# Optimization experiments

Hardware: AMD Instinct MI355X
Metric: run time of the kernel (lower is better)

## Reference

```python
import jax, jax.numpy as jnp
import numpy as np

H = 256        # hidden_channels
G = 13         # num_input_geofeature
E = 100000     # number of 2nd-order triplets
N = 50000      # num_nodes
DEPTH = 3      # finaldepth
EPS = 1e-5     # BatchNorm eps


def setup_inputs() -> dict:
    key = jax.random.key(0)
    ks = jax.random.split(key, 10)
    d_in = 3 * H + G  # 781
    return {
        "node_feature": jax.random.normal(ks[0], (N, H), jnp.float32),
        "geo_encoding": jax.random.normal(ks[1], (E, G), jnp.float32),
        "edge_index_2rd": jax.random.randint(ks[2], (3, E), 0, N),
        "edx_ij": jax.random.randint(ks[3], (E,), 0, 2 * E),
        "edx_jk": jax.random.randint(ks[4], (E,), 0, 2 * E),
        "att": jax.random.uniform(ks[5], (4,), jnp.float32),
        # 4 branches: layer0 (d_in->H) + DEPTH layers (H->H), xavier-ish init, zero bias
        "W0": jax.random.normal(ks[6], (4, d_in, H), jnp.float32) * (1.0 / np.sqrt(d_in)),
        "b0": jnp.zeros((4, H), jnp.float32),
        "Wh": jax.random.normal(ks[7], (4, DEPTH, H, H), jnp.float32) * (1.0 / np.sqrt(H)),
        "bh": jnp.zeros((4, DEPTH, H), jnp.float32),
        # BatchNorm (eval mode): affine params + running stats, one per layer per branch
        "gamma": jnp.ones((4, DEPTH + 1, H), jnp.float32),
        "beta": jnp.zeros((4, DEPTH + 1, H), jnp.float32),
        "run_mean": jnp.zeros((4, DEPTH + 1, H), jnp.float32),
        "run_var": jnp.ones((4, DEPTH + 1, H), jnp.float32),
        "num_edge_inside": E,
        "num_nodes": N,
    }


def _bn(h, g, b, m, v):
    return (h - m) * jax.lax.rsqrt(v + EPS) * g + b


def reference(node_feature, geo_encoding, edge_index_2rd, edx_ij, edx_jk, att,
              W0, b0, Wh, bh, gamma, beta, run_mean, run_var,
              num_edge_inside, num_nodes):
    i, j, k = edge_index_2rd[0], edge_index_2rd[1], edge_index_2rd[2]
    # gather node triplets + geo features -> [E, 3H+G]
    x = jnp.concatenate(
        [node_feature[i], node_feature[j], node_feature[k], geo_encoding], axis=-1)

    m_ij = edx_ij < num_edge_inside
    m_jk = edx_jk < num_edge_inside
    # 4 mutually-exclusive, exhaustive routing masks: [4, E]
    masks = jnp.stack([m_ij & m_jk, m_ij & ~m_jk, ~m_ij & m_jk, ~m_ij & ~m_jk])

    x_output = jnp.zeros((x.shape[0], H), x.dtype)
    for br in range(4):  # fixed small branch count
        h = jax.nn.relu(_bn(x @ W0[br] + b0[br],
                            gamma[br, 0], beta[br, 0], run_mean[br, 0], run_var[br, 0]))
        for l in range(DEPTH):
            h = jax.nn.relu(_bn(h @ Wh[br, l] + bh[br, l],
                                gamma[br, l + 1], beta[br, l + 1],
                                run_mean[br, l + 1], run_var[br, l + 1]))
        h = jax.nn.leaky_relu(h) * att[br]
        x_output = x_output + jnp.where(masks[br][:, None], h, jnp.zeros((), h.dtype))
    # scatter_add over target node index i -> [num_nodes, H]
    return jax.ops.segment_sum(x_output, i, num_segments=num_nodes)
```

## Files before the change

### kernel.cpp

```cpp
#include <hip/hip_runtime.h>
#include <hip/hip_bf16.h>
#include <stdint.h>

#define HCH 256
#define GEO 13
#define DEPTH 3
#define EPSBN 1e-5f
#define MFMA __builtin_amdgcn_mfma_f32_16x16x32_bf16

typedef __attribute__((ext_vector_type(8))) short short8;
typedef __attribute__((ext_vector_type(4))) float floatx4;

__device__ __forceinline__ short f2bs(float f) {
    unsigned u = __float_as_uint(f);
    unsigned r = (u + 0x7fffu + ((u >> 16) & 1u)) >> 16;
    return (short)r;
}

__global__ void k_prep(const float* __restrict__ W0, const float* __restrict__ Wh,
                       const float* __restrict__ b0, const float* __restrict__ bh,
                       const float* __restrict__ gm, const float* __restrict__ bt,
                       const float* __restrict__ mn, const float* __restrict__ vr,
                       const float* __restrict__ att,
                       const float* __restrict__ node, const float* __restrict__ geo,
                       const int* __restrict__ edx_ij, const int* __restrict__ edx_jk,
                       const int* __restrict__ nei_p,
                       short* __restrict__ W0t, short* __restrict__ Wht,
                       float* __restrict__ sc, float* __restrict__ of,
                       short* __restrict__ node_bf, short* __restrict__ geo_bf,
                       int* __restrict__ lists, int* __restrict__ cnt,
                       float4* __restrict__ outz, int n4out,
                       int E, int d_in_dim, int nb_node, int nb_geo, int nb_out) {
    const int B_W0 = 100, B_WH = 96, B_SC = 16;
    __shared__ short s[32][256];
    int b = blockIdx.x, t = threadIdx.x;
    if (b < B_W0) {
        int c = b % 25, br = b / 25;
        #pragma unroll
        for (int kk = 0; kk < 32; ++kk) {
            int kidx = c * 32 + kk;
            float v = (kidx < d_in_dim) ? W0[((size_t)br * d_in_dim + kidx) * HCH + t] : 0.f;
            s[kk][t] = f2bs(v);
        }
        __syncthreads();
        size_t obase = ((size_t)(b) * 256 + t) * 32;
        #pragma unroll
        for (int g = 0; g < 4; ++g) {
            short8 v;
            #pragma unroll
            for (int j = 0; j < 8; ++j) v[j] = s[g * 8 + j][t];
            *reinterpret_cast<short8*>(W0t + obase + g * 8) = v;
        }
    } else if (b < B_W0 + B_WH) {
        int idx = b - B_W0;
        int c = idx & 7; idx >>= 3;
        int l = idx % 3, br = idx / 3;
        #pragma unroll
        for (int kk = 0; kk < 32; ++kk) {
            float v = Wh[((size_t)(br * DEPTH + l) * HCH + (c * 32 + kk)) * HCH + t];
            s[kk][t] = f2bs(v);
        }
        __syncthreads();
        size_t obase = ((size_t)(b - B_W0) * 256 + t) * 32;
        #pragma unroll
        for (int g = 0; g < 4; ++g) {
            short8 v;
            #pragma unroll
            for (int j = 0; j < 8; ++j) v[j] = s[g * 8 + j][t];
            *reinterpret_cast<short8*>(Wht + obase + g * 8) = v;
        }
    } else if (b < B_W0 + B_WH + B_SC) {
        int idx = (b - B_W0 - B_WH) * 256 + t;
        int col = idx & 255, l = (idx >> 8) & 3, br = idx >> 10;
        int gi = (br * (DEPTH + 1) + l) * HCH + col;
        float sA = gm[gi] * rsqrtf(vr[gi] + EPSBN);
        float bias = (l == 0) ? b0[br * HCH + col] : bh[(br * DEPTH + (l - 1)) * HCH + col];
        float ofv = (bias - mn[gi]) * sA + bt[gi];
        if (l == 3) { float av = att[br]; sA *= av; ofv *= av; }
        sc[idx] = sA;
        of[idx] = ofv;
    } else if (b < B_W0 + B_WH + B_SC + nb_node) {
        size_t i = ((size_t)(b - B_W0 - B_WH - B_SC) * 256 + t) * 8;
        const float4* src = reinterpret_cast<const float4*>(node + i);
        float4 v0 = src[0], v1 = src[1];
        short8 pk;
        pk[0] = f2bs(v0.x); pk[1] = f2bs(v0.y); pk[2] = f2bs(v0.z); pk[3] = f2bs(v0.w);
        pk[4] = f2bs(v1.x); pk[5] = f2bs(v1.y); pk[6] = f2bs(v1.z); pk[7] = f2bs(v1.w);
        *reinterpret_cast<short8*>(node_bf + i) = pk;
    } else if (b < B_W0 + B_WH + B_SC + nb_node + nb_geo) {
        int i = (b - B_W0 - B_WH - B_SC - nb_node) * 256 + t;
        int e = i >> 2, cc = i & 3;
        if (e < E) {
            short8 pk;
            #pragma unroll
            for (int j = 0; j < 8; ++j) {
                int col = cc * 8 + j;
                pk[j] = (col < GEO) ? f2bs(geo[(size_t)e * GEO + col]) : (short)0;
            }
            *reinterpret_cast<short8*>(geo_bf + (size_t)e * 32 + cc * 8) = pk;
        }
    } else if (b < B_W0 + B_WH + B_SC + nb_node + nb_geo + nb_out) {
        int i = (b - (B_W0 + B_WH + B_SC + nb_node + nb_geo)) * 256 + t;
        if (i < n4out) outz[i] = make_float4(0.f, 0.f, 0.f, 0.f);
    } else {
        int e = (b - (B_W0 + B_WH + B_SC + nb_node + nb_geo + nb_out)) * 256 + t;
        int NEI = nei_p[0];
        int lane = t & 63;
        int br = -1;
        if (e < E)
            br = ((edx_ij[e] < NEI) ? 0 : 2) + ((edx_jk[e] < NEI) ? 0 : 1);
        unsigned long long lt = (lane == 63) ? 0x7fffffffffffffffull
                                             : ((1ull << lane) - 1ull);
        #pragma unroll
        for (int bb = 0; bb < 4; ++bb) {
            unsigned long long mk = __ballot(br == bb);
            if (mk) {
                int leader = __ffsll((long long)mk) - 1;
                int base = 0;
                if (lane == leader) base = atomicAdd(&cnt[bb], (int)__popcll(mk));
                base = __shfl(base, leader);
                if (br == bb) {
                    int pos = base + (int)__popcll(mk & lt);
                    lists[(size_t)bb * E + pos] = e;
                }
            }
        }
    }
}

__global__ __launch_bounds__(512)
void k_main(const short* __restrict__ node_bf, const short* __restrict__ geo_bf,
            const int* __restrict__ eidx,
            const short* __restrict__ W0t, const short* __restrict__ Wht,
            const float* __restrict__ sc, const float* __restrict__ of,
            const int* __restrict__ lists, const int* __restrict__ cnt,
            float* __restrict__ out, int E) {
    __shared__ __align__(16) short A[64][256];
    __shared__ __align__(16) short Ageo[64][40];
    __shared__ int s_idx[3][64];
    __shared__ int s_e[64];

    int c0 = cnt[0], c1 = cnt[1], c2 = cnt[2], c3 = cnt[3];
    int t0 = (c0 + 63) >> 6, t1 = (c1 + 63) >> 6, t2 = (c2 + 63) >> 6, t3 = (c3 + 63) >> 6;
    int b = blockIdx.x;
    int br, tile, count;
    if (b < t0)                     { br = 0; tile = b;                count = c0; }
    else if (b < t0 + t1)           { br = 1; tile = b - t0;           count = c1; }
    else if (b < t0 + t1 + t2)      { br = 2; tile = b - t0 - t1;      count = c2; }
    else if (b < t0 + t1 + t2 + t3) { br = 3; tile = b - t0 - t1 - t2; count = c3; }
    else return;
    int m = count - tile * 64; if (m > 64) m = 64;

    int t = threadIdx.x;
    if (t < 64) {
        int e = (t < m) ? lists[(size_t)br * E + (size_t)tile * 64 + t] : 0;
        s_e[t] = (t < m) ? e : -1;
        s_idx[0][t] = eidx[e];
        s_idx[1][t] = eidx[E + e];
        s_idx[2][t] = eidx[2 * E + e];
    }
    __syncthreads();

    int wv = t >> 6, lane = t & 63, quad = lane >> 4, l16 = lane & 15;
    int rbase = t >> 5, cc8 = (t & 31) * 8;
    int swz = (l16 & 7) << 4;

    floatx4 acc[4][2];
    #pragma unroll
    for (int rt = 0; rt < 4; ++rt)
        #pragma unroll
        for (int ct = 0; ct < 2; ++ct)
            #pragma unroll
            for (int r = 0; r < 4; ++r) acc[rt][ct][r] = 0.f;

    int boff[2];
    #pragma unroll
    for (int ct = 0; ct < 2; ++ct)
        boff[ct] = (wv * 32 + ct * 16 + l16) * 32 + quad * 8;

    const char* Ab = (const char*)&A[0][0];
    char* Aw = (char*)&A[0][0];
    short* Ag = &Ageo[0][0];

    auto do_chunks8 = [&](const short* Wbase) {
        short8 bb[4][2];
        #pragma unroll
        for (int s = 0; s < 3; ++s)
            #pragma unroll
            for (int ct = 0; ct < 2; ++ct)
                bb[s][ct] = *reinterpret_cast<const short8*>(
                    Wbase + (size_t)s * 8192 + boff[ct]);
        #pragma unroll
        for (int c = 0; c < 8; ++c) {
            if (c + 3 < 8) {
                const short* Bn = Wbase + (size_t)(c + 3) * 8192;
                #pragma unroll
                for (int ct = 0; ct < 2; ++ct)
                    bb[(c + 3) & 3][ct] = *reinterpret_cast<const short8*>(Bn + boff[ct]);
            }
            short8 af[4];
            #pragma unroll
            for (int rt = 0; rt < 4; ++rt)
                af[rt] = *reinterpret_cast<const short8*>(
                    Ab + (rt * 16 + l16) * 512 + ((c * 64 + quad * 16) ^ swz));
            __builtin_amdgcn_s_setprio(1);
            #pragma unroll
            for (int rt = 0; rt < 4; ++rt)
                #pragma unroll
                for (int ct = 0; ct < 2; ++ct)
                    acc[rt][ct] = MFMA(af[rt], bb[c & 3][ct], acc[rt][ct], 0, 0, 0);
            __builtin_amdgcn_s_setprio(0);
        }
    };
    auto do_chunk1 = [&](const short* Wbase) {
        short8 bc[2];
        #pragma unroll
        for (int ct = 0; ct < 2; ++ct)
            bc[ct] = *reinterpret_cast<const short8*>(Wbase + boff[ct]);
        short8 af[4];
        #pragma unroll
        for (int rt = 0; rt < 4; ++rt)
            af[rt] = *reinterpret_cast<const short8*>(
                Ag + (rt * 16 + l16) * 40 + quad * 8);
        __builtin_amdgcn_s_setprio(1);
        #pragma unroll
        for (int rt = 0; rt < 4; ++rt)
            #pragma unroll
            for (int ct = 0; ct < 2; ++ct)
                acc[rt][ct] = MFMA(af[rt], bc[ct], acc[rt][ct], 0, 0, 0);
        __builtin_amdgcn_s_setprio(0);
    };

    if (t < 256) {
        int grow = t >> 2, gp = (t & 3) * 8;
        int ge = s_e[grow];
        short8 gv;
        if (ge >= 0) gv = *reinterpret_cast<const short8*>(geo_bf + (size_t)ge * 32 + gp);
        else {
            #pragma unroll
            for (int j = 0; j < 8; ++j) gv[j] = 0;
        }
        *reinterpret_cast<short8*>(Ag + grow * 40 + gp) = gv;
    }
    short8 g[2][4];
    #pragma unroll
    for (int it = 0; it < 4; ++it)
        g[0][it] = *reinterpret_cast<const short8*>(
            node_bf + (size_t)s_idx[0][it * 16 + rbase] * HCH + cc8);

    #pragma unroll
    for (int p = 0; p < 3; ++p) {
        __syncthreads();
        #pragma unroll
        for (int it = 0; it < 4; ++it) {
            int row = it * 16 + rbase;
            *reinterpret_cast<short8*>(
                Aw + row * 512 + ((cc8 * 2) ^ ((row & 7) << 4))) = g[p & 1][it];
        }
        __syncthreads();
        if (p < 2) {
            const int* idxs = s_idx[p + 1];
            #pragma unroll
            for (int it = 0; it < 4; ++it)
                g[(p + 1) & 1][it] = *reinterpret_cast<const short8*>(
                    node_bf + (size_t)idxs[it * 16 + rbase] * HCH + cc8);
        }
        do_chunks8(W0t + (size_t)(br * 25 + p * 8) * 8192);
    }
    do_chunk1(W0t + (size_t)(br * 25 + 24) * 8192);

    for (int l = 0; l < 4; ++l) {
        float sv[2], ov[2];
        #pragma unroll
        for (int ct = 0; ct < 2; ++ct) {
            int col = wv * 32 + ct * 16 + l16;
            sv[ct] = sc[(br * 4 + l) * HCH + col];
            ov[ct] = of[(br * 4 + l) * HCH + col];
        }
        if (l < 3) {
            __syncthreads();
            #pragma unroll
            for (int rt = 0; rt < 4; ++rt)
                #pragma unroll
                for (int ct = 0; ct < 2; ++ct) {
                    int colb = (wv * 32 + ct * 16 + l16) * 2;
                    #pragma unroll
                    for (int r = 0; r < 4; ++r) {
                        int row = rt * 16 + quad * 4 + r;
                        float h = fmaxf(acc[rt][ct][r] * sv[ct] + ov[ct], 0.f);
                        *reinterpret_cast<short*>(
                            Aw + row * 512 + (colb ^ ((row & 7) << 4))) = f2bs(h);
                        acc[rt][ct][r] = 0.f;
                    }
                }
            __syncthreads();
            do_chunks8(Wht + (size_t)((br * 3 + l) * 8) * 8192);
        } else {
            #pragma unroll
            for (int rt = 0; rt < 4; ++rt)
                #pragma unroll
                for (int r = 0; r < 4; ++r) {
                    int row = rt * 16 + quad * 4 + r;
                    if (row < m) {
                        float* orow = out + (size_t)s_idx[0][row] * HCH + wv * 32 + l16;
                        #pragma unroll
                        for (int ct = 0; ct < 2; ++ct) {
                            float h = fmaxf(acc[rt][ct][r] * sv[ct] + ov[ct], 0.f);
                            atomicAdd(orow + ct * 16, h);
                        }
                    }
                }
        }
    }
}

extern "C" void kernel_launch(void* const* d_in, const int* in_sizes, int n_in,
                              void* d_out, int out_size, void* d_ws, size_t ws_size,
                              hipStream_t stream) {
    const float* node  = (const float*)d_in[0];
    const float* geo   = (const float*)d_in[1];
    const int*   eidx  = (const int*)d_in[2];
    const int*   edxij = (const int*)d_in[3];
    const int*   edxjk = (const int*)d_in[4];
    const float* att   = (const float*)d_in[5];
    const float* W0    = (const float*)d_in[6];
    const float* b0    = (const float*)d_in[7];
    const float* Wh    = (const float*)d_in[8];
    const float* bh    = (const float*)d_in[9];
    const float* gm    = (const float*)d_in[10];
    const float* bt    = (const float*)d_in[11];
    const float* mn    = (const float*)d_in[12];
    const float* vr    = (const float*)d_in[13];
    const int*   neip  = (const int*)d_in[14];

    int E = in_sizes[3];
    int N = in_sizes[0] / HCH;
    int d_in_dim = in_sizes[6] / (4 * HCH);

    uint8_t* w = (uint8_t*)d_ws;
    size_t off = 0;
    short* W0t  = (short*)(w + off); off += (size_t)4 * 25 * 256 * 32 * 2;
    short* Wht  = (short*)(w + off); off += (size_t)4 * 3 * 8 * 256 * 32 * 2;
    float* sc   = (float*)(w + off); off += 4096 * 4;
    float* of   = (float*)(w + off); off += 4096 * 4;
    int*   lists= (int*)(w + off);   off += (size_t)4 * E * 4;
    int*   cnt  = (int*)(w + off);   off += 16;
    short* node_bf = (short*)(w + off); off += (size_t)N * HCH * 2;
    short* geo_bf  = (short*)(w + off); off += (size_t)E * 32 * 2;

    float* out = (float*)d_out;
    int n4 = out_size / 4;

    hipMemsetAsync(cnt, 0, 16, stream);

    int nb_node = N / 8;
    int nb_geo  = (4 * E + 255) / 256;
    int nb_out  = (n4 + 255) / 256;
    int nb_cmp  = (E + 255) / 256;
    k_prep<<<100 + 96 + 16 + nb_node + nb_geo + nb_out + nb_cmp, 256, 0, stream>>>(
        W0, Wh, b0, bh, gm, bt, mn, vr, att, node, geo, edxij, edxjk, neip,
        W0t, Wht, sc, of, node_bf, geo_bf, lists, cnt,
        (float4*)out, n4, E, d_in_dim, nb_node, nb_geo, nb_out);

    int T = (E >> 6) + 8;
    k_main<<<T, 512, 0, stream>>>(node_bf, geo_bf, eidx, W0t, Wht,
                                  sc, of, lists, cnt, out, E);
}
```

Measured before the change: 409.4 us.

## Pad LDS rows instead of XOR swizzle, remap blocks per XCD, trim prefetch

Replaces the XOR-swizzled shared-memory layout for the activation tile with a padded row stride of 264 shorts. Block IDs are remapped so that consecutive logical tiles land on the same XCD, which is meant to improve L2 locality for weights and branch data. The weight prefetch depth in the chunk loop drops from three to two buffers, and the MFMA priority hints are removed. Padding adds a little LDS, and the shallower prefetch may expose more global load latency.

New measurement: 393.7 us. 1.04x faster.

```diff
diff --git a/kernel.cpp b/kernel.cpp
--- a/kernel.cpp
+++ b/kernel.cpp
@@ -135,14 +135,18 @@
             const float* __restrict__ sc, const float* __restrict__ of,
             const int* __restrict__ lists, const int* __restrict__ cnt,
             float* __restrict__ out, int E) {
-    __shared__ __align__(16) short A[64][256];
+    __shared__ __align__(16) short A[64][264];
     __shared__ __align__(16) short Ageo[64][40];
     __shared__ int s_idx[3][64];
     __shared__ int s_e[64];
 
+    int nwg = gridDim.x;
+    int q = nwg >> 3, r = nwg & 7;
+    int xcd = blockIdx.x & 7, jj = blockIdx.x >> 3;
+    int b = ((xcd < r) ? xcd * (q + 1) : r * (q + 1) + (xcd - r) * q) + jj;
+
     int c0 = cnt[0], c1 = cnt[1], c2 = cnt[2], c3 = cnt[3];
     int t0 = (c0 + 63) >> 6, t1 = (c1 + 63) >> 6, t2 = (c2 + 63) >> 6, t3 = (c3 + 63) >> 6;
-    int b = blockIdx.x;
     int br, tile, count;
     if (b < t0)                     { br = 0; tile = b;                count = c0; }
     else if (b < t0 + t1)           { br = 1; tile = b - t0;           count = c1; }
@@ -163,7 +167,6 @@
 
     int wv = t >> 6, lane = t & 63, quad = lane >> 4, l16 = lane & 15;
     int rbase = t >> 5, cc8 = (t & 31) * 8;
-    int swz = (l16 & 7) << 4;
 
     floatx4 acc[4][2];
     #pragma unroll
@@ -171,45 +174,39 @@
         #pragma unroll
         for (int ct = 0; ct < 2; ++ct)
             #pragma unroll
-            for (int r = 0; r < 4; ++r) acc[rt][ct][r] = 0.f;
+            for (int r2 = 0; r2 < 4; ++r2) acc[rt][ct][r2] = 0.f;
 
     int boff[2];
     #pragma unroll
     for (int ct = 0; ct < 2; ++ct)
         boff[ct] = (wv * 32 + ct * 16 + l16) * 32 + quad * 8;
 
-    const char* Ab = (const char*)&A[0][0];
-    char* Aw = (char*)&A[0][0];
     short* Ag = &Ageo[0][0];
 
     auto do_chunks8 = [&](const short* Wbase) {
-        short8 bb[4][2];
-        #pragma unroll
-        for (int s = 0; s < 3; ++s)
-            #pragma unroll
-            for (int ct = 0; ct < 2; ++ct)
-                bb[s][ct] = *reinterpret_cast<const short8*>(
-                    Wbase + (size_t)s * 8192 + boff[ct]);
+        short8 bb[3][2];
+        #pragma unroll
+        for (int ct = 0; ct < 2; ++ct) {
+            bb[0][ct] = *reinterpret_cast<const short8*>(Wbase + boff[ct]);
+            bb[1][ct] = *reinterpret_cast<const short8*>(Wbase + 8192 + boff[ct]);
+        }
         #pragma unroll
         for (int c = 0; c < 8; ++c) {
-            if (c + 3 < 8) {
-                const short* Bn = Wbase + (size_t)(c + 3) * 8192;
+            if (c + 2 < 8) {
+                const short* Bn = Wbase + (size_t)(c + 2) * 8192;
                 #pragma unroll
                 for (int ct = 0; ct < 2; ++ct)
-                    bb[(c + 3) & 3][ct] = *reinterpret_cast<const short8*>(Bn + boff[ct]);
+                    bb[(c + 2) % 3][ct] = *reinterpret_cast<const short8*>(Bn + boff[ct]);
             }
             short8 af[4];
             #pragma unroll
             for (int rt = 0; rt < 4; ++rt)
-                af[rt] = *reinterpret_cast<const short8*>(
-                    Ab + (rt * 16 + l16) * 512 + ((c * 64 + quad * 16) ^ swz));
-            __builtin_amdgcn_s_setprio(1);
+                af[rt] = *reinterpret_cast<const short8*>(&A[rt * 16 + l16][c * 32 + quad * 8]);
             #pragma unroll
             for (int rt = 0; rt < 4; ++rt)
                 #pragma unroll
                 for (int ct = 0; ct < 2; ++ct)
-                    acc[rt][ct] = MFMA(af[rt], bb[c & 3][ct], acc[rt][ct], 0, 0, 0);
-            __builtin_amdgcn_s_setprio(0);
+                    acc[rt][ct] = MFMA(af[rt], bb[c % 3][ct], acc[rt][ct], 0, 0, 0);
         }
     };
     auto do_chunk1 = [&](const short* Wbase) {
@@ -220,15 +217,12 @@
         short8 af[4];
         #pragma unroll
         for (int rt = 0; rt < 4; ++rt)
-            af[rt] = *reinterpret_cast<const short8*>(
-                Ag + (rt * 16 + l16) * 40 + quad * 8);
-        __builtin_amdgcn_s_setprio(1);
+            af[rt] = *reinterpret_cast<const short8*>(Ag + (rt * 16 + l16) * 40 + quad * 8);
         #pragma unroll
         for (int rt = 0; rt < 4; ++rt)
             #pragma unroll
             for (int ct = 0; ct < 2; ++ct)
                 acc[rt][ct] = MFMA(af[rt], bc[ct], acc[rt][ct], 0, 0, 0);
-        __builtin_amdgcn_s_setprio(0);
     };
 
     if (t < 256) {
@@ -252,11 +246,8 @@
     for (int p = 0; p < 3; ++p) {
         __syncthreads();
         #pragma unroll
-        for (int it = 0; it < 4; ++it) {
-            int row = it * 16 + rbase;
-            *reinterpret_cast<short8*>(
-                Aw + row * 512 + ((cc8 * 2) ^ ((row & 7) << 4))) = g[p & 1][it];
-        }
+        for (int it = 0; it < 4; ++it)
+            *reinterpret_cast<short8*>(&A[it * 16 + rbase][cc8]) = g[p & 1][it];
         __syncthreads();
         if (p < 2) {
             const int* idxs = s_idx[p + 1];
@@ -283,14 +274,13 @@
             for (int rt = 0; rt < 4; ++rt)
                 #pragma unroll
                 for (int ct = 0; ct < 2; ++ct) {
-                    int colb = (wv * 32 + ct * 16 + l16) * 2;
+                    int col = wv * 32 + ct * 16 + l16;
                     #pragma unroll
-                    for (int r = 0; r < 4; ++r) {
-                        int row = rt * 16 + quad * 4 + r;
-                        float h = fmaxf(acc[rt][ct][r] * sv[ct] + ov[ct], 0.f);
-                        *reinterpret_cast<short*>(
-                            Aw + row * 512 + (colb ^ ((row & 7) << 4))) = f2bs(h);
-                        acc[rt][ct][r] = 0.f;
+                    for (int r2 = 0; r2 < 4; ++r2) {
+                        int row = rt * 16 + quad * 4 + r2;
+                        float h = fmaxf(acc[rt][ct][r2] * sv[ct] + ov[ct], 0.f);
+                        A[row][col] = f2bs(h);
+                        acc[rt][ct][r2] = 0.f;
                     }
                 }
             __syncthreads();
@@ -299,13 +289,13 @@
             #pragma unroll
             for (int rt = 0; rt < 4; ++rt)
                 #pragma unroll
-                for (int r = 0; r < 4; ++r) {
-                    int row = rt * 16 + quad * 4 + r;
+                for (int r2 = 0; r2 < 4; ++r2) {
+                    int row = rt * 16 + quad * 4 + r2;
                     if (row < m) {
                         float* orow = out + (size_t)s_idx[0][row] * HCH + wv * 32 + l16;
                         #pragma unroll
                         for (int ct = 0; ct < 2; ++ct) {
-                            float h = fmaxf(acc[rt][ct][r] * sv[ct] + ov[ct], 0.f);
+                            float h = fmaxf(acc[rt][ct][r2] * sv[ct] + ov[ct], 0.f);
                             atomicAdd(orow + ct * 16, h);
                         }
                     }
```
